# Performance work log

Hardware: AMD Instinct MI355X
Metric: run time of the kernel (lower is better)

## Reference

```python
import jax, jax.numpy as jnp
import numpy as np

B, N, C, H, NH, NC = 4, 2048, 256, 128, 8, 3  # batch, points, in_ch, hidden, heads, classes
DH = H // NH


def setup_inputs() -> dict:
    key = jax.random.key(0)
    ki = iter(jax.random.split(key, 48))
    def w(shape, s=0.05):
        return jax.random.normal(next(ki), shape, jnp.float32) * s
    z = lambda n: jnp.zeros((n,), jnp.float32)
    o = lambda n: jnp.ones((n,), jnp.float32)
    inp = dict(x=jax.random.normal(next(ki), (B, N, C), jnp.float32))
    inp.update(fuse_w1=w((H, C)), fuse_b1=z(H), fuse_w2=w((H, H)), fuse_b2=z(H))
    for l in range(2):
        inp[f'attn{l}_in_w'] = w((3 * H, H)); inp[f'attn{l}_in_b'] = z(3 * H)
        inp[f'attn{l}_out_w'] = w((H, H)); inp[f'attn{l}_out_b'] = z(H)
        inp[f'ffn{l}_w1'] = w((2 * H, H)); inp[f'ffn{l}_b1'] = z(2 * H)
        inp[f'ffn{l}_w2'] = w((H, 2 * H)); inp[f'ffn{l}_b2'] = z(H)
        inp[f'ln{2*l}_g'] = o(H); inp[f'ln{2*l}_b'] = z(H)
        inp[f'ln{2*l+1}_g'] = o(H); inp[f'ln{2*l+1}_b'] = z(H)
    inp.update(out_w1=w((H, H)), out_b1=z(H), out_w2=w((NC, H)), out_b2=z(NC))
    inp.update(det_w1=w((H // 2, H)), det_b1=z(H // 2), det_w2=w((1, H // 2)), det_b2=z(1))
    return inp


def _ln(x, g, b):
    m = jnp.mean(x, axis=-1, keepdims=True)
    v = jnp.mean((x - m) ** 2, axis=-1, keepdims=True)
    return (x - m) * jax.lax.rsqrt(v + 1e-5) * g + b


def _mha(x, in_w, in_b, out_w, out_b):
    # nn.MultiheadAttention (batch_first, self-attn), eval mode (no dropout)
    Bq, Nq, _ = x.shape
    qkv = x @ in_w.T + in_b                          # [B,N,3H]
    q, k, v = jnp.split(qkv, 3, axis=-1)
    q = q.reshape(Bq, Nq, NH, DH)
    k = k.reshape(Bq, Nq, NH, DH)
    v = v.reshape(Bq, Nq, NH, DH)
    s = jnp.einsum('bqhd,bkhd->bhqk', q, k) / jnp.sqrt(jnp.float32(DH))
    a = jax.nn.softmax(s, axis=-1)
    o = jnp.einsum('bhqk,bkhd->bqhd', a, v).reshape(Bq, Nq, H)
    return o @ out_w.T + out_b


def _forward(x, fuse_w1, fuse_b1, fuse_w2, fuse_b2,
             attn0_in_w, attn0_in_b, attn0_out_w, attn0_out_b,
             ffn0_w1, ffn0_b1, ffn0_w2, ffn0_b2, ln0_g, ln0_b, ln1_g, ln1_b,
             attn1_in_w, attn1_in_b, attn1_out_w, attn1_out_b,
             ffn1_w1, ffn1_b1, ffn1_w2, ffn1_b2, ln2_g, ln2_b, ln3_g, ln3_b,
             out_w1, out_b1, out_w2, out_b2, det_w1, det_b1, det_w2, det_b2):
    # feature_fusion (dropout = identity in eval)
    h = jnp.maximum(x @ fuse_w1.T + fuse_b1, 0) @ fuse_w2.T + fuse_b2
    layers = [
        (attn0_in_w, attn0_in_b, attn0_out_w, attn0_out_b, ffn0_w1, ffn0_b1, ffn0_w2, ffn0_b2, ln0_g, ln0_b, ln1_g, ln1_b),
        (attn1_in_w, attn1_in_b, attn1_out_w, attn1_out_b, ffn1_w1, ffn1_b1, ffn1_w2, ffn1_b2, ln2_g, ln2_b, ln3_g, ln3_b),
    ]
    for (iw, ib, ow, ob, f1w, f1b, f2w, f2b, g1, be1, g2, be2) in layers:
        h = _ln(h + _mha(h, iw, ib, ow, ob), g1, be1)
        h = _ln(h + (jnp.maximum(h @ f1w.T + f1b, 0) @ f2w.T + f2b), g2, be2)
    refined_logits = jnp.maximum(h @ out_w1.T + out_b1, 0) @ out_w2.T + out_b2   # [B,N,NC]
    head_prob = jax.nn.sigmoid(jnp.maximum(h @ det_w1.T + det_b1, 0) @ det_w2.T + det_b2)[..., 0]  # [B,N]
    quality = jnp.mean(head_prob, axis=1)                                        # [B]
    return refined_logits, head_prob, quality


def reference(x, fuse_w1, fuse_b1, fuse_w2, fuse_b2,
              attn0_in_w, attn0_in_b, attn0_out_w, attn0_out_b,
              ffn0_w1, ffn0_b1, ffn0_w2, ffn0_b2, ln0_g, ln0_b, ln1_g, ln1_b,
              attn1_in_w, attn1_in_b, attn1_out_w, attn1_out_b,
              ffn1_w1, ffn1_b1, ffn1_w2, ffn1_b2, ln2_g, ln2_b, ln3_g, ln3_b,
              out_w1, out_b1, out_w2, out_b2, det_w1, det_b1, det_w2, det_b2):
    return _forward(x, fuse_w1, fuse_b1, fuse_w2, fuse_b2,
                    attn0_in_w, attn0_in_b, attn0_out_w, attn0_out_b,
                    ffn0_w1, ffn0_b1, ffn0_w2, ffn0_b2, ln0_g, ln0_b, ln1_g, ln1_b,
                    attn1_in_w, attn1_in_b, attn1_out_w, attn1_out_b,
                    ffn1_w1, ffn1_b1, ffn1_w2, ffn1_b2, ln2_g, ln2_b, ln3_g, ln3_b,
                    out_w1, out_b1, out_w2, out_b2, det_w1, det_b1, det_w2, det_b2)
```

## Files before the change

### kernel.cpp

```cpp
#include <hip/hip_runtime.h>
#include <cstddef>

constexpr int Bb  = 4;
constexpr int Nn  = 2048;
constexpr int Cc  = 256;
constexpr int Hh  = 128;
constexpr int NHh = 8;
constexpr int DHh = 16;
constexpr int MTOK = Bb * Nn;
#define LOG2E 1.4426950408889634f

typedef __attribute__((ext_vector_type(8))) short bf16x8;
typedef __attribute__((ext_vector_type(4))) short bf16x4;
typedef __attribute__((ext_vector_type(4))) float f32x4;

__device__ __forceinline__ short f32_to_bf16_rne(float f) {
    union { float f; unsigned int u; } c; c.f = f;
    unsigned int r = c.u + 0x7fffu + ((c.u >> 16) & 1u);
    return (short)(r >> 16);
}
__device__ __forceinline__ float bf16_to_f32(short s) {
    union { float f; unsigned int u; } c; c.u = ((unsigned int)(unsigned short)s) << 16;
    return c.f;
}
__device__ __forceinline__ unsigned pack2_bf16(float a, float b) {
    unsigned ua = __float_as_uint(a);
    unsigned ub = __float_as_uint(b);
    ua += 0x7fffu + ((ua >> 16) & 1u);
    ub += 0x7fffu + ((ub >> 16) & 1u);
    return __builtin_amdgcn_perm(ub, ua, 0x07060302);
}

struct CvtJobs {
    const float* src[13];
    short*       dst[13];
    int          off[14];
    float*       qzero;
};

__global__ __launch_bounds__(256) void cvt_kernel(CvtJobs j) {
    const int gid = blockIdx.x * 256 + threadIdx.x;
    if (blockIdx.x == 0 && threadIdx.x < 4) j.qzero[threadIdx.x] = 0.f;
    if (gid >= j.off[13]) return;
    int k = 0;
    #pragma unroll
    for (int i = 0; i < 12; ++i) if (gid >= j.off[i + 1]) k = i + 1;
    const int idx = (gid - j.off[k]) * 4;
    float4 v = *(const float4*)(j.src[k] + idx);
    short o4[4] = { f32_to_bf16_rne(v.x), f32_to_bf16_rne(v.y),
                    f32_to_bf16_rne(v.z), f32_to_bf16_rne(v.w) };
    *(bf16x4*)(j.dst[k] + idx) = *(bf16x4*)o4;
}

__global__ __launch_bounds__(256) void gemm_bf16_kernel(
    const short* __restrict__ X, const short* __restrict__ W,
    const float* __restrict__ bias, short* __restrict__ Yb,
    int M, int N, int K, int relu)
{
    __shared__ short As[64 * 40];
    __shared__ short Bs[64 * 40];

    const int tid  = threadIdx.x;
    const int lane = tid & 63;
    const int wv   = tid >> 6;
    const int col  = lane & 15;
    const int g    = lane >> 4;
    const int m0   = blockIdx.y * 64;
    const int n0   = blockIdx.x * 64;
    const int sr   = tid >> 2;
    const int sc   = (tid & 3) * 8;

    f32x4 acc[4] = {};

    for (int k0 = 0; k0 < K; k0 += 32) {
        __syncthreads();
        *(bf16x8*)&As[sr * 40 + sc] =
            *(const bf16x8*)(X + (size_t)(m0 + sr) * K + k0 + sc);
        *(bf16x8*)&Bs[sr * 40 + sc] =
            *(const bf16x8*)(W + (size_t)(n0 + sr) * K + k0 + sc);
        __syncthreads();

        bf16x8 a = *(bf16x8*)&As[(wv * 16 + col) * 40 + g * 8];
        #pragma unroll
        for (int jj = 0; jj < 4; ++jj) {
            bf16x8 b = *(bf16x8*)&Bs[(jj * 16 + col) * 40 + g * 8];
            acc[jj] = __builtin_amdgcn_mfma_f32_16x16x32_bf16(a, b, acc[jj], 0, 0, 0);
        }
    }

    #pragma unroll
    for (int jj = 0; jj < 4; ++jj) {
        const int cn = n0 + jj * 16 + col;
        const float bb = bias[cn];
        #pragma unroll
        for (int r = 0; r < 4; ++r) {
            const int rm = m0 + wv * 16 + g * 4 + r;
            float v = acc[jj][r] + bb;
            if (relu) v = fmaxf(v, 0.f);
            Yb[(size_t)rm * N + cn] = f32_to_bf16_rne(v);
        }
    }
}

template<int K, int CR, bool DO_LN>
__global__ __launch_bounds__(256) void gemmln_kernel(
    const short* __restrict__ X, const short* __restrict__ W,
    const float* __restrict__ bias,
    float* __restrict__ hf, short* __restrict__ hb,
    const float* __restrict__ gw, const float* __restrict__ bw)
{
    constexpr int ST  = K + 8;
    constexpr int NCH = 128 / CR;
    constexpr int NF  = CR / 32;
    __shared__ short As[32 * ST];
    __shared__ short Ws[CR * ST];
    __shared__ float P[32 * 130];

    const int tid  = threadIdx.x;
    const int lane = tid & 63;
    const int wv   = tid >> 6;
    const int col  = lane & 15;
    const int g    = lane >> 4;
    const int m0   = blockIdx.x * 32;
    const int mst  = (wv & 1) * 16;
    const int cb   = (wv >> 1) * (CR / 2);

    for (int i = tid; i < 32 * (K / 8); i += 256) {
        const int r = i / (K / 8), c = (i % (K / 8)) * 8;
        *(bf16x8*)&As[r * ST + c] = *(const bf16x8*)(X + (size_t)(m0 + r) * K + c);
    }

    f32x4 ya[NCH][NF] = {};
    #pragma unroll
    for (int ch = 0; ch < NCH; ++ch) {
        for (int i = tid; i < CR * (K / 8); i += 256) {
            const int r = i / (K / 8), c = (i % (K / 8)) * 8;
            *(bf16x8*)&Ws[r * ST + c] =
                *(const bf16x8*)(W + (size_t)(ch * CR + r) * K + c);
        }
        __syncthreads();
        #pragma unroll
        for (int k0 = 0; k0 < K; k0 += 32) {
            bf16x8 a = *(bf16x8*)&As[(mst + col) * ST + k0 + g * 8];
            #pragma unroll
            for (int f = 0; f < NF; ++f) {
                bf16x8 b = *(bf16x8*)&Ws[(cb + f * 16 + col) * ST + k0 + g * 8];
                ya[ch][f] = __builtin_amdgcn_mfma_f32_16x16x32_bf16(a, b, ya[ch][f], 0, 0, 0);
            }
        }
        __syncthreads();
    }

    #pragma unroll
    for (int ch = 0; ch < NCH; ++ch)
        #pragma unroll
        for (int f = 0; f < NF; ++f) {
            const int cn = ch * CR + cb + f * 16 + col;
            const float bb = bias[cn];
            #pragma unroll
            for (int r = 0; r < 4; ++r)
                P[(mst + g * 4 + r) * 130 + cn] = ya[ch][f][r] + bb;
        }
    __syncthreads();

    #pragma unroll
    for (int rr = 0; rr < 8; ++rr) {
        const int row = wv * 8 + rr;
        const size_t t = m0 + row;
        float2 pv = *(float2*)&P[row * 130 + 2 * lane];
        if (DO_LN) {
            float2 hv = ((const float2*)(hf + t * Hh))[lane];
            float a0 = hv.x + pv.x, a1 = hv.y + pv.y;
            float sum = a0 + a1;
            #pragma unroll
            for (int off = 32; off > 0; off >>= 1) sum += __shfl_xor(sum, off);
            const float mean = sum * (1.f / 128.f);
            const float d0 = a0 - mean, d1 = a1 - mean;
            float vs = d0 * d0 + d1 * d1;
            #pragma unroll
            for (int off = 32; off > 0; off >>= 1) vs += __shfl_xor(vs, off);
            const float rstd = rsqrtf(vs * (1.f / 128.f) + 1e-5f);
            float2 gv = ((const float2*)gw)[lane];
            float2 bv = ((const float2*)bw)[lane];
            float2 r = { d0 * rstd * gv.x + bv.x, d1 * rstd * gv.y + bv.y };
            ((float2*)(hf + t * Hh))[lane] = r;
            *(unsigned*)&hb[t * Hh + lane * 2] = pack2_bf16(r.x, r.y);
        } else {
            ((float2*)(hf + t * Hh))[lane] = pv;
            *(unsigned*)&hb[t * Hh + lane * 2] = pack2_bf16(pv.x, pv.y);
        }
    }
}

template<int K, int MID, int CR1, int CR2, bool DO_LN>
__global__ __launch_bounds__(256) void mlp2_kernel(
    const short* __restrict__ X,
    const short* __restrict__ W1, const float* __restrict__ b1,
    const short* __restrict__ W2, const float* __restrict__ b2,
    float* __restrict__ hf, short* __restrict__ hb,
    const float* __restrict__ gw, const float* __restrict__ bw)
{
    constexpr int STA = K + 8;
    constexpr int STU = MID + 8;
    constexpr int WS1 = CR1 * STA;
    constexpr int WS2 = CR2 * STU;
    constexpr int WSZ = (WS1 > WS2) ? WS1 : WS2;
    __shared__ short As[32 * STA];
    __shared__ short Ws[WSZ];
    __shared__ short U[32 * STU];
    __shared__ float P[32 * 130];

    const int tid  = threadIdx.x;
    const int lane = tid & 63;
    const int wv   = tid >> 6;
    const int col  = lane & 15;
    const int g    = lane >> 4;
    const int m0   = blockIdx.x * 32;
    const int mst  = (wv & 1) * 16;

    for (int i = tid; i < 32 * (K / 8); i += 256) {
        const int r = i / (K / 8), c = (i % (K / 8)) * 8;
        *(bf16x8*)&As[r * STA + c] = *(const bf16x8*)(X + (size_t)(m0 + r) * K + c);
    }

    constexpr int NCH1 = MID / CR1;
    constexpr int NF1  = CR1 / 32;
    const int cb1 = (wv >> 1) * (CR1 / 2);
    #pragma unroll
    for (int ch = 0; ch < NCH1; ++ch) {
        for (int i = tid; i < CR1 * (K / 8); i += 256) {
            const int r = i / (K / 8), c = (i % (K / 8)) * 8;
            *(bf16x8*)&Ws[r * STA + c] =
                *(const bf16x8*)(W1 + (size_t)(ch * CR1 + r) * K + c);
        }
        __syncthreads();
        f32x4 ya[NF1] = {};
        #pragma unroll
        for (int k0 = 0; k0 < K; k0 += 32) {
            bf16x8 a = *(bf16x8*)&As[(mst + col) * STA + k0 + g * 8];
            #pragma unroll
            for (int f = 0; f < NF1; ++f) {
                bf16x8 b = *(bf16x8*)&Ws[(cb1 + f * 16 + col) * STA + k0 + g * 8];
                ya[f] = __builtin_amdgcn_mfma_f32_16x16x32_bf16(a, b, ya[f], 0, 0, 0);
            }
        }
        #pragma unroll
        for (int f = 0; f < NF1; ++f) {
            const int cn = ch * CR1 + cb1 + f * 16 + col;
            const float bb = b1[cn];
            #pragma unroll
            for (int r = 0; r < 4; ++r)
                U[(mst + g * 4 + r) * STU + cn] =
                    f32_to_bf16_rne(fmaxf(ya[f][r] + bb, 0.f));
        }
        __syncthreads();
    }

    constexpr int NCH2 = 128 / CR2;
    constexpr int NF2  = CR2 / 32;
    const int cb2 = (wv >> 1) * (CR2 / 2);
    f32x4 yb[NCH2][NF2] = {};
    #pragma unroll
    for (int ch = 0; ch < NCH2; ++ch) {
        for (int i = tid; i < CR2 * (MID / 8); i += 256) {
            const int r = i / (MID / 8), c = (i % (MID / 8)) * 8;
            *(bf16x8*)&Ws[r * STU + c] =
                *(const bf16x8*)(W2 + (size_t)(ch * CR2 + r) * MID + c);
        }
        __syncthreads();
        #pragma unroll
        for (int k0 = 0; k0 < MID; k0 += 32) {
            bf16x8 a = *(bf16x8*)&U[(mst + col) * STU + k0 + g * 8];
            #pragma unroll
            for (int f = 0; f < NF2; ++f) {
                bf16x8 b = *(bf16x8*)&Ws[(cb2 + f * 16 + col) * STU + k0 + g * 8];
                yb[ch][f] = __builtin_amdgcn_mfma_f32_16x16x32_bf16(a, b, yb[ch][f], 0, 0, 0);
            }
        }
        __syncthreads();
    }

    #pragma unroll
    for (int ch = 0; ch < NCH2; ++ch)
        #pragma unroll
        for (int f = 0; f < NF2; ++f) {
            const int cn = ch * CR2 + cb2 + f * 16 + col;
            const float bb = b2[cn];
            #pragma unroll
            for (int r = 0; r < 4; ++r)
                P[(mst + g * 4 + r) * 130 + cn] = yb[ch][f][r] + bb;
        }
    __syncthreads();

    #pragma unroll
    for (int rr = 0; rr < 8; ++rr) {
        const int row = wv * 8 + rr;
        const size_t t = m0 + row;
        float2 pv = *(float2*)&P[row * 130 + 2 * lane];
        if (DO_LN) {
            float2 hv = ((const float2*)(hf + t * Hh))[lane];
            float a0 = hv.x + pv.x, a1 = hv.y + pv.y;
            float sum = a0 + a1;
            #pragma unroll
            for (int off = 32; off > 0; off >>= 1) sum += __shfl_xor(sum, off);
            const float mean = sum * (1.f / 128.f);
            const float d0 = a0 - mean, d1 = a1 - mean;
            float vs = d0 * d0 + d1 * d1;
            #pragma unroll
            for (int off = 32; off > 0; off >>= 1) vs += __shfl_xor(vs, off);
            const float rstd = rsqrtf(vs * (1.f / 128.f) + 1e-5f);
            float2 gv = ((const float2*)gw)[lane];
            float2 bv = ((const float2*)bw)[lane];
            float2 r = { d0 * rstd * gv.x + bv.x, d1 * rstd * gv.y + bv.y };
            ((float2*)(hf + t * Hh))[lane] = r;
            *(unsigned*)&hb[t * Hh + lane * 2] = pack2_bf16(r.x, r.y);
        } else {
            ((float2*)(hf + t * Hh))[lane] = pv;
            *(unsigned*)&hb[t * Hh + lane * 2] = pack2_bf16(pv.x, pv.y);
        }
    }
}

__global__ __launch_bounds__(256) void head_kernel(
    const short* __restrict__ X,
    const short* __restrict__ W1b, const float* __restrict__ b1,
    const short* __restrict__ DW1b, const float* __restrict__ db1,
    const float* __restrict__ w2, const float* __restrict__ b2,
    const float* __restrict__ dw2, const float* __restrict__ db2,
    float* __restrict__ out)
{
    constexpr int K = 128, ST = K + 8;
    __shared__ short As[32 * ST];
    __shared__ short Ws[64 * ST];
    __shared__ float P[32 * 196];

    const int tid  = threadIdx.x;
    const int lane = tid & 63;
    const int wv   = tid >> 6;
    const int col  = lane & 15;
    const int g    = lane >> 4;
    const int m0   = blockIdx.x * 32;
    const int mst  = (wv & 1) * 16;
    const int cb   = (wv >> 1) * 32;

    for (int i = tid; i < 32 * (K / 8); i += 256) {
        const int r = i / (K / 8), c = (i % (K / 8)) * 8;
        *(bf16x8*)&As[r * ST + c] = *(const bf16x8*)(X + (size_t)(m0 + r) * K + c);
    }

    f32x4 ya[3][2] = {};
    #pragma unroll
    for (int ch = 0; ch < 3; ++ch) {
        for (int i = tid; i < 64 * (K / 8); i += 256) {
            const int r = i / (K / 8), c = (i % (K / 8)) * 8;
            const int rg = ch * 64 + r;
            const short* src = (rg < 128) ? (W1b + (size_t)rg * K)
                                          : (DW1b + (size_t)(rg - 128) * K);
            *(bf16x8*)&Ws[r * ST + c] = *(const bf16x8*)(src + c);
        }
        __syncthreads();
        #pragma unroll
        for (int k0 = 0; k0 < K; k0 += 32) {
            bf16x8 a = *(bf16x8*)&As[(mst + col) * ST + k0 + g * 8];
            #pragma unroll
            for (int f = 0; f < 2; ++f) {
                bf16x8 b = *(bf16x8*)&Ws[(cb + f * 16 + col) * ST + k0 + g * 8];
                ya[ch][f] = __builtin_amdgcn_mfma_f32_16x16x32_bf16(a, b, ya[ch][f], 0, 0, 0);
            }
        }
        __syncthreads();
    }

    #pragma unroll
    for (int ch = 0; ch < 3; ++ch)
        #pragma unroll
        for (int f = 0; f < 2; ++f) {
            const int cn = ch * 64 + cb + f * 16 + col;
            const float bb = (cn < 128) ? b1[cn] : db1[cn - 128];
            #pragma unroll
            for (int r = 0; r < 4; ++r)
                P[(mst + g * 4 + r) * 196 + cn] = fmaxf(ya[ch][f][r] + bb, 0.f);
        }
    __syncthreads();

    const float w20 = w2[2 * lane],       w21 = w2[2 * lane + 1];
    const float w22 = w2[128 + 2 * lane], w23 = w2[129 + 2 * lane];
    const float w24 = w2[256 + 2 * lane], w25 = w2[257 + 2 * lane];
    const float dwl = dw2[lane];
    float qacc = 0.f;
    #pragma unroll
    for (int rr = 0; rr < 8; ++rr) {
        const int row = wv * 8 + rr;
        const size_t t = m0 + row;
        const float x0 = P[row * 196 + 2 * lane];
        const float x1 = P[row * 196 + 2 * lane + 1];
        float s0 = x0 * w20 + x1 * w21;
        float s1 = x0 * w22 + x1 * w23;
        float s2 = x0 * w24 + x1 * w25;
        float d  = P[row * 196 + 128 + lane] * dwl;
        #pragma unroll
        for (int off = 32; off > 0; off >>= 1) {
            s0 += __shfl_xor(s0, off);
            s1 += __shfl_xor(s1, off);
            s2 += __shfl_xor(s2, off);
            d  += __shfl_xor(d,  off);
        }
        if (lane == 0) {
            out[t * 3 + 0] = s0 + b2[0];
            out[t * 3 + 1] = s1 + b2[1];
            out[t * 3 + 2] = s2 + b2[2];
            const float prob = 1.f / (1.f + __expf(-(d + db2[0])));
            out[24576 + t] = prob;
            qacc += prob;
        }
    }
    if (lane == 0)
        atomicAdd(&out[32768 + (m0 >> 11)], qacc * (1.f / (float)Nn));
}

constexpr int KT = 128;
constexpr int KS = 28;
constexpr int VS = 132;

__global__ __launch_bounds__(256) void attn_kernel(
    const short* __restrict__ qkv, short* __restrict__ out)
{
    __shared__ short Ks[KT * KS];
    __shared__ short Vs[DHh * VS];

    const int tid  = threadIdx.x;
    const int lane = tid & 63;
    const int wv   = tid >> 6;
    const int col  = lane & 15;
    const int g    = lane >> 4;
    const int hd   = blockIdx.y;
    const int b    = blockIdx.z;
    const int q0   = blockIdx.x * 64 + wv * 16;

    const short* base = qkv + (size_t)b * Nn * 384;

    bf16x8 qf = {};
    if (g < 2) {
        bf16x8 qraw = *(const bf16x8*)(base + (size_t)(q0 + col) * 384 + hd * DHh + g * 8);
        const float qs = 0.25f * LOG2E;
        #pragma unroll
        for (int i = 0; i < 8; ++i)
            qf[i] = f32_to_bf16_rne(bf16_to_f32(qraw[i]) * qs);
    }

    f32x4 o    = {0.f, 0.f, 0.f, 0.f};
    f32x4 lacc = {0.f, 0.f, 0.f, 0.f};
    const short one_bf16 = (short)0x3F80;
    const bf16x8 ones = { one_bf16, one_bf16, one_bf16, one_bf16,
                          one_bf16, one_bf16, one_bf16, one_bf16 };

    const int ksr = tid >> 1;
    const int ksd = (tid & 1) * 8;
    const int va  = tid >> 2;
    const int vd  = (tid & 3) * 4;

    for (int kt = 0; kt < Nn; kt += KT) {
        __syncthreads();
        {
            *(bf16x8*)&Ks[ksr * KS + ksd] =
                *(const bf16x8*)(base + (size_t)(kt + ksr) * 384 + Hh + hd * DHh + ksd);
            const short* v0 = base + (size_t)(kt + 2 * va) * 384 + 2 * Hh + hd * DHh + vd;
            bf16x4 r0 = *(const bf16x4*)v0;
            bf16x4 r1 = *(const bf16x4*)(v0 + 384);
            unsigned a0 = ((const unsigned*)&r0)[0], a1 = ((const unsigned*)&r0)[1];
            unsigned b0 = ((const unsigned*)&r1)[0], b1 = ((const unsigned*)&r1)[1];
            *(unsigned*)&Vs[(vd + 0) * VS + 2 * va] = __builtin_amdgcn_perm(b0, a0, 0x05040100);
            *(unsigned*)&Vs[(vd + 1) * VS + 2 * va] = __builtin_amdgcn_perm(b0, a0, 0x07060302);
            *(unsigned*)&Vs[(vd + 2) * VS + 2 * va] = __builtin_amdgcn_perm(b1, a1, 0x05040100);
            *(unsigned*)&Vs[(vd + 3) * VS + 2 * va] = __builtin_amdgcn_perm(b1, a1, 0x07060302);
        }
        __syncthreads();

        #pragma unroll
        for (int s = 0; s < 4; ++s) {
            bf16x8 kf0 = {}, kf1 = {};
            if (g < 2) {
                kf0 = *(bf16x8*)&Ks[(s * 32 + col) * KS + g * 8];
                kf1 = *(bf16x8*)&Ks[(s * 32 + 16 + col) * KS + g * 8];
            }
            f32x4 z = {0.f, 0.f, 0.f, 0.f};
            f32x4 sA = __builtin_amdgcn_mfma_f32_16x16x32_bf16(kf0, qf, z, 0, 0, 0);
            f32x4 sB = __builtin_amdgcn_mfma_f32_16x16x32_bf16(kf1, qf, z, 0, 0, 0);

            union { bf16x8 v; unsigned u[4]; } pf;
            pf.u[0] = pack2_bf16(__builtin_amdgcn_exp2f(sA[0]),
                                 __builtin_amdgcn_exp2f(sA[1]));
            pf.u[1] = pack2_bf16(__builtin_amdgcn_exp2f(sA[2]),
                                 __builtin_amdgcn_exp2f(sA[3]));
            pf.u[2] = pack2_bf16(__builtin_amdgcn_exp2f(sB[0]),
                                 __builtin_amdgcn_exp2f(sB[1]));
            pf.u[3] = pack2_bf16(__builtin_amdgcn_exp2f(sB[2]),
                                 __builtin_amdgcn_exp2f(sB[3]));

            bf16x8 vf;
            ((bf16x4*)&vf)[0] = *(bf16x4*)&Vs[col * VS + s * 32 + g * 4];
            ((bf16x4*)&vf)[1] = *(bf16x4*)&Vs[col * VS + s * 32 + 16 + g * 4];

            o    = __builtin_amdgcn_mfma_f32_16x16x32_bf16(pf.v, vf,   o,    0, 0, 0);
            lacc = __builtin_amdgcn_mfma_f32_16x16x32_bf16(pf.v, ones, lacc, 0, 0, 0);
        }
    }

    #pragma unroll
    for (int r = 0; r < 4; ++r) {
        const float inv = __builtin_amdgcn_rcpf(lacc[r]);
        out[(size_t)(b * Nn + q0 + g * 4 + r) * Hh + hd * DHh + col] =
            f32_to_bf16_rne(o[r] * inv);
    }
}

extern "C" void kernel_launch(void* const* d_in, const int* in_sizes, int n_in,
                              void* d_out, int out_size, void* d_ws, size_t ws_size,
                              hipStream_t stream)
{
    char* W8 = (char*)d_ws;
    float* hf   = (float*)(W8 + 0);
    short* hb   = (short*)(W8 + 4194304);
    short* wb   = (short*)(W8 + 6291456);
    char*  regA = W8 + 7340032;
    char*  regB = W8 + 13631488;

    short* xb    = (short*)regA;
    short* qkvb  = (short*)regA;
    short* attno = (short*)regB;
    float* out   = (float*)d_out;

    const int wsz[12]  = {32768,16384,49152,16384,32768,32768,49152,16384,32768,32768,16384,8192};
    const int wsrc[12] = {1, 3, 5, 7, 9, 11, 17, 19, 21, 23, 29, 33};
    int woff[13]; woff[0] = 0;
    for (int i = 0; i < 12; ++i) woff[i + 1] = woff[i] + wsz[i];

    CvtJobs jobs;
    int acc = 0;
    for (int i = 0; i < 12; ++i) {
        jobs.src[i] = (const float*)d_in[wsrc[i]];
        jobs.dst[i] = wb + woff[i];
        jobs.off[i] = acc;
        acc += wsz[i] / 4;
    }
    jobs.src[12] = (const float*)d_in[0];
    jobs.dst[12] = xb;
    jobs.off[12] = acc;
    acc += (MTOK * Cc) / 4;
    jobs.off[13] = acc;
    jobs.qzero = out + 32768;

    hipLaunchKernelGGL(cvt_kernel, dim3((acc + 255) / 256), dim3(256), 0, stream, jobs);

    hipLaunchKernelGGL((mlp2_kernel<256, 128, 32, 64, false>), dim3(MTOK / 32), dim3(256), 0,
                       stream, xb, wb + woff[0], (const float*)d_in[2],
                       wb + woff[1], (const float*)d_in[4], hf, hb, nullptr, nullptr);

    for (int l = 0; l < 2; ++l) {
        const int ib = 5 + l * 12;
        const int wbase = 2 + l * 4;
        hipLaunchKernelGGL(gemm_bf16_kernel, dim3(384 / 64, MTOK / 64), dim3(256), 0, stream,
                           hb, wb + woff[wbase + 0], (const float*)d_in[ib + 1], qkvb,
                           MTOK, 3 * Hh, Hh, 0);
        hipLaunchKernelGGL(attn_kernel, dim3(Nn / 64, NHh, Bb), dim3(256), 0, stream,
                           qkvb, attno);
        hipLaunchKernelGGL((gemmln_kernel<128, 64, true>), dim3(MTOK / 32), dim3(256), 0, stream,
                           attno, wb + woff[wbase + 1], (const float*)d_in[ib + 3],
                           hf, hb, (const float*)d_in[ib + 8], (const float*)d_in[ib + 9]);
        hipLaunchKernelGGL((mlp2_kernel<128, 256, 64, 32, true>), dim3(MTOK / 32), dim3(256), 0,
                           stream, hb, wb + woff[wbase + 2], (const float*)d_in[ib + 5],
                           wb + woff[wbase + 3], (const float*)d_in[ib + 7],
                           hf, hb, (const float*)d_in[ib + 10], (const float*)d_in[ib + 11]);
    }

    hipLaunchKernelGGL(head_kernel, dim3(MTOK / 32), dim3(256), 0, stream,
                       hb, wb + woff[10], (const float*)d_in[30],
                       wb + woff[11], (const float*)d_in[34],
                       (const float*)d_in[31], (const float*)d_in[32],
                       (const float*)d_in[35], (const float*)d_in[36], out);
}
```

Measured before the change: 299.5 us.

## Split attention over key chunks with a separate reduction kernel

Splits each attention block's key loop into four independent chunks, launching four times as many blocks. Each chunk writes its unnormalised fp32 output and row-sum partials to workspace. A new reduce kernel sums the partials, normalises and writes bf16 output. This is meant to raise parallelism and occupancy across CUs, at the cost of about 16 MB of extra fp32 workspace traffic per layer and one extra launch.

```diff
diff --git a/kernel.cpp b/kernel.cpp
--- a/kernel.cpp
+++ b/kernel.cpp
@@ -421,9 +421,12 @@
 constexpr int KT = 128;
 constexpr int KS = 28;
 constexpr int VS = 132;
+constexpr int NSPLIT = 4;
+constexpr int KCH = Nn / NSPLIT;
 
 __global__ __launch_bounds__(256) void attn_kernel(
-    const short* __restrict__ qkv, short* __restrict__ out)
+    const short* __restrict__ qkv, float* __restrict__ o_ws,
+    float* __restrict__ l_ws)
 {
     __shared__ short Ks[KT * KS];
     __shared__ short Vs[DHh * VS];
@@ -435,7 +438,9 @@
     const int g    = lane >> 4;
     const int hd   = blockIdx.y;
     const int b    = blockIdx.z;
-    const int q0   = blockIdx.x * 64 + wv * 16;
+    const int sp   = blockIdx.x & (NSPLIT - 1);
+    const int qb   = blockIdx.x >> 2;
+    const int q0   = qb * 64 + wv * 16;
 
     const short* base = qkv + (size_t)b * Nn * 384;
 
@@ -459,7 +464,7 @@
     const int va  = tid >> 2;
     const int vd  = (tid & 3) * 4;
 
-    for (int kt = 0; kt < Nn; kt += KT) {
+    for (int kt = sp * KCH; kt < (sp + 1) * KCH; kt += KT) {
         __syncthreads();
         {
             *(bf16x8*)&Ks[ksr * KS + ksd] =
@@ -508,10 +513,30 @@
 
     #pragma unroll
     for (int r = 0; r < 4; ++r) {
-        const float inv = __builtin_amdgcn_rcpf(lacc[r]);
-        out[(size_t)(b * Nn + q0 + g * 4 + r) * Hh + hd * DHh + col] =
-            f32_to_bf16_rne(o[r] * inv);
-    }
+        const size_t t = (size_t)b * Nn + q0 + g * 4 + r;
+        o_ws[((size_t)sp * MTOK + t) * Hh + hd * DHh + col] = o[r];
+        if (col == 0)
+            l_ws[((size_t)sp * MTOK + t) * NHh + hd] = lacc[r];
+    }
+}
+
+__global__ __launch_bounds__(256) void attn_reduce_kernel(
+    const float* __restrict__ o_ws, const float* __restrict__ l_ws,
+    short* __restrict__ attno)
+{
+    const int gid = blockIdx.x * 256 + threadIdx.x;
+    const int t   = gid >> 6;
+    const int dp  = (gid & 63) * 2;
+    const int hd  = dp >> 4;
+    float ox = 0.f, oy = 0.f, ls = 0.f;
+    #pragma unroll
+    for (int sp = 0; sp < NSPLIT; ++sp) {
+        float2 ov = *(const float2*)&o_ws[((size_t)sp * MTOK + t) * Hh + dp];
+        ox += ov.x; oy += ov.y;
+        ls += l_ws[((size_t)sp * MTOK + t) * NHh + hd];
+    }
+    const float inv = __builtin_amdgcn_rcpf(ls);
+    *(unsigned*)&attno[(size_t)t * Hh + dp] = pack2_bf16(ox * inv, oy * inv);
 }
 
 extern "C" void kernel_launch(void* const* d_in, const int* in_sizes, int n_in,
@@ -524,6 +549,8 @@
     short* wb   = (short*)(W8 + 6291456);
     char*  regA = W8 + 7340032;
     char*  regB = W8 + 13631488;
+    float* o_ws = (float*)(W8 + 16777216);
+    float* l_ws = (float*)(W8 + 33554432);
 
     short* xb    = (short*)regA;
     short* qkvb  = (short*)regA;
@@ -562,8 +589,10 @@
         hipLaunchKernelGGL(gemm_bf16_kernel, dim3(384 / 64, MTOK / 64), dim3(256), 0, stream,
                            hb, wb + woff[wbase + 0], (const float*)d_in[ib + 1], qkvb,
                            MTOK, 3 * Hh, Hh, 0);
-        hipLaunchKernelGGL(attn_kernel, dim3(Nn / 64, NHh, Bb), dim3(256), 0, stream,
-                           qkvb, attno);
+        hipLaunchKernelGGL(attn_kernel, dim3((Nn / 64) * NSPLIT, NHh, Bb), dim3(256), 0,
+                           stream, qkvb, o_ws, l_ws);
+        hipLaunchKernelGGL(attn_reduce_kernel, dim3(MTOK * 64 / 256), dim3(256), 0, stream,
+                           o_ws, l_ws, attno);
         hipLaunchKernelGGL((gemmln_kernel<128, 64, true>), dim3(MTOK / 32), dim3(256), 0, stream,
                            attno, wb + woff[wbase + 1], (const float*)d_in[ib + 3],
                            hf, hb, (const float*)d_in[ib + 8], (const float*)d_in[ib + 9]);
```

Result: slower. 308.7 us (+3.1%).

## Store QKV in head-major layout so attention loads contiguous per-head tiles

Applied to the files above, without the earlier changes.

The QKV projection GEMM now writes its output as three separate [B, heads, N, 16] sections instead of a token-major [tokens, 384] row layout, and K, N are fixed at compile time. The attention kernel reads Q, K and V from these contiguous per-head regions, so each key/value tile load covers dense memory instead of 32-byte pieces strided by 768 bytes. The cost is a scattered store pattern in the GEMM epilogue, where each 2-byte write lands in a different 32-byte row.

```diff
diff --git a/kernel.cpp b/kernel.cpp
--- a/kernel.cpp
+++ b/kernel.cpp
@@ -52,11 +52,11 @@
     *(bf16x4*)(j.dst[k] + idx) = *(bf16x4*)o4;
 }
 
-__global__ __launch_bounds__(256) void gemm_bf16_kernel(
+__global__ __launch_bounds__(256) void gemm_qkv_kernel(
     const short* __restrict__ X, const short* __restrict__ W,
-    const float* __restrict__ bias, short* __restrict__ Yb,
-    int M, int N, int K, int relu)
+    const float* __restrict__ bias, short* __restrict__ Yb)
 {
+    constexpr int K = 128, N = 384;
     __shared__ short As[64 * 40];
     __shared__ short Bs[64 * 40];
 
@@ -90,14 +90,18 @@
 
     #pragma unroll
     for (int jj = 0; jj < 4; ++jj) {
-        const int cn = n0 + jj * 16 + col;
+        const int cn  = n0 + jj * 16 + col;
+        const int sec = cn >> 7;
+        const int hd  = (cn & 127) >> 4;
+        const int d   = cn & 15;
         const float bb = bias[cn];
         #pragma unroll
         for (int r = 0; r < 4; ++r) {
             const int rm = m0 + wv * 16 + g * 4 + r;
+            const int bq = rm >> 11, tt = rm & 2047;
             float v = acc[jj][r] + bb;
-            if (relu) v = fmaxf(v, 0.f);
-            Yb[(size_t)rm * N + cn] = f32_to_bf16_rne(v);
+            Yb[(size_t)sec * (MTOK * 128)
+               + ((size_t)(bq * NHh + hd) * Nn + tt) * DHh + d] = f32_to_bf16_rne(v);
         }
     }
 }
@@ -437,11 +441,14 @@
     const int b    = blockIdx.z;
     const int q0   = blockIdx.x * 64 + wv * 16;
 
-    const short* base = qkv + (size_t)b * Nn * 384;
+    const size_t bh = (size_t)(b * NHh + hd) * Nn * DHh;
+    const short* Qh = qkv + bh;
+    const short* Kh = qkv + (size_t)MTOK * 128 + bh;
+    const short* Vh = qkv + (size_t)2 * MTOK * 128 + bh;
 
     bf16x8 qf = {};
     if (g < 2) {
-        bf16x8 qraw = *(const bf16x8*)(base + (size_t)(q0 + col) * 384 + hd * DHh + g * 8);
+        bf16x8 qraw = *(const bf16x8*)(Qh + (size_t)(q0 + col) * DHh + g * 8);
         const float qs = 0.25f * LOG2E;
         #pragma unroll
         for (int i = 0; i < 8; ++i)
@@ -463,10 +470,10 @@
         __syncthreads();
         {
             *(bf16x8*)&Ks[ksr * KS + ksd] =
-                *(const bf16x8*)(base + (size_t)(kt + ksr) * 384 + Hh + hd * DHh + ksd);
-            const short* v0 = base + (size_t)(kt + 2 * va) * 384 + 2 * Hh + hd * DHh + vd;
+                *(const bf16x8*)(Kh + (size_t)(kt + ksr) * DHh + ksd);
+            const short* v0 = Vh + (size_t)(kt + 2 * va) * DHh + vd;
             bf16x4 r0 = *(const bf16x4*)v0;
-            bf16x4 r1 = *(const bf16x4*)(v0 + 384);
+            bf16x4 r1 = *(const bf16x4*)(v0 + DHh);
             unsigned a0 = ((const unsigned*)&r0)[0], a1 = ((const unsigned*)&r0)[1];
             unsigned b0 = ((const unsigned*)&r1)[0], b1 = ((const unsigned*)&r1)[1];
             *(unsigned*)&Vs[(vd + 0) * VS + 2 * va] = __builtin_amdgcn_perm(b0, a0, 0x05040100);
@@ -559,9 +566,8 @@
     for (int l = 0; l < 2; ++l) {
         const int ib = 5 + l * 12;
         const int wbase = 2 + l * 4;
-        hipLaunchKernelGGL(gemm_bf16_kernel, dim3(384 / 64, MTOK / 64), dim3(256), 0, stream,
-                           hb, wb + woff[wbase + 0], (const float*)d_in[ib + 1], qkvb,
-                           MTOK, 3 * Hh, Hh, 0);
+        hipLaunchKernelGGL(gemm_qkv_kernel, dim3(384 / 64, MTOK / 64), dim3(256), 0, stream,
+                           hb, wb + woff[wbase + 0], (const float*)d_in[ib + 1], qkvb);
         hipLaunchKernelGGL(attn_kernel, dim3(Nn / 64, NHh, Bb), dim3(256), 0, stream,
                            qkvb, attno);
         hipLaunchKernelGGL((gemmln_kernel<128, 64, true>), dim3(MTOK / 32), dim3(256), 0, stream,
```

New measurement: 299.9 us. Within noise of the previous version (+0.1%).
